# Optimization experiments

Hardware: AMD Instinct MI355X
Metric: run time of the kernel (lower is better)

## Reference

```python
import jax, jax.numpy as jnp
import numpy as np

D_MODEL = 1024

def setup_inputs() -> dict:
    key = jax.random.key(0)
    k1, k2, kU, kb, kw, kfb = jax.random.split(key, 6)
    B, S, d = 8, 2048, D_MODEL
    x1 = jax.random.normal(k1, (B, S, d), dtype=jnp.float32)
    x2 = jax.random.normal(k2, (B, S, d), dtype=jnp.float32)
    U = jax.random.normal(kU, (d, d), dtype=jnp.float32) * (1.0 / np.sqrt(d))
    bias = jax.random.normal(kb, (d,), dtype=jnp.float32) * 0.02
    fc_w = jax.random.normal(kw, (d // 2, d), dtype=jnp.float32) * (1.0 / np.sqrt(d))
    fc_b = jnp.zeros((d // 2,), dtype=jnp.float32)
    return {"x1": x1, "x2": x2, "U": U, "bias": bias, "fc_w": fc_w, "fc_b": fc_b}

def reference(x1, x2, U, bias, fc_w, fc_b):
    # attn scores: (x2 @ U) @ x1^T  -> [B, S2, S1]
    attn = jnp.einsum("bsd,de,bte->bst", x2, U, x1)
    # additive bias per key position: x1 @ bias -> [B, 1, S1]
    attn = attn + jnp.einsum("btd,d->bt", x1, bias)[:, None, :]
    attn = jax.nn.softmax(attn, axis=-1)
    # dropout is identity in eval mode
    out = jnp.einsum("bst,btd->bsd", attn, x1)
    out = jnp.einsum("bsd,ed->bse", out, fc_w) + fc_b
    return jax.nn.relu(out)
```

## Files before the change

### kernel.cpp

```cpp
#include <hip/hip_runtime.h>
#include <hip/hip_fp16.h>
#include <cstddef>
#include <cstdint>

typedef _Float16 f16;
typedef _Float16 f16x8 __attribute__((ext_vector_type(8)));
typedef _Float16 f16x4 __attribute__((ext_vector_type(4)));
typedef float    f32x4 __attribute__((ext_vector_type(4)));

#define BK 64

__device__ __forceinline__ void gload16(const void* g, void* lds) {
  __builtin_amdgcn_global_load_lds(
      (const __attribute__((address_space(1))) unsigned int*)g,
      (__attribute__((address_space(3))) unsigned int*)lds, 16, 0, 0);
}

template<int R>
__device__ __forceinline__ void stage_f16(f16 (*buf)[BK], const f16* __restrict__ src,
                                          int ld, int w, int lane) {
#pragma unroll
  for (int i = 0; i < R / 32; i++) {
    const int grp  = w * (R / 32) + i;
    const int r    = grp * 8 + (lane >> 3);
    const int slot = (lane & 7) ^ (r & 7);
    gload16(src + (size_t)r * ld + slot * 8, &buf[grp * 8][0]);
  }
}

template<int R>
struct RegStage {
  static constexpr int NV = (R == 128) ? 8 : 4;
  float4 v[NV];
  __device__ __forceinline__ void load(const float* __restrict__ src, int ld, int tid) {
    const int r = (R == 128) ? (tid >> 1) : (tid >> 2);
    const int h = (R == 128) ? (tid & 1) * 32 : (tid & 3) * 16;
    const float* p = src + (size_t)r * ld + h;
#pragma unroll
    for (int j = 0; j < NV; j++) v[j] = ((const float4*)p)[j];
  }
  __device__ __forceinline__ void write(f16 (*buf)[BK], int tid) {
    const int r = (R == 128) ? (tid >> 1) : (tid >> 2);
    const int h = (R == 128) ? (tid & 1) * 32 : (tid & 3) * 16;
#pragma unroll
    for (int g = 0; g < NV / 2; g++) {
      const float4 a = v[g * 2], b = v[g * 2 + 1];
      f16x8 o;
      o[0] = (f16)a.x; o[1] = (f16)a.y; o[2] = (f16)a.z; o[3] = (f16)a.w;
      o[4] = (f16)b.x; o[5] = (f16)b.y; o[6] = (f16)b.z; o[7] = (f16)b.w;
      const int slot = (h / 8 + g) ^ (r & 7);
      *(f16x8*)&buf[r][slot * 8] = o;
    }
  }
};

template<int BMt, int BNt, typename TA, typename TB, bool BIAS, bool RELU, typename TC>
__global__ __launch_bounds__(256, 2)
void gemm_tn(const TA* __restrict__ A, int lda,
             const TB* __restrict__ B, int ldb,
             TC* __restrict__ C, int ldc,
             const float* __restrict__ bias, int K)
{
  constexpr int MF = BMt / 32;
  constexpr int NF = BNt / 32;
  __shared__ f16 As[2][BMt][BK];
  __shared__ f16 Bs[2][BNt][BK];
  const int tid  = threadIdx.x;
  const int lane = tid & 63;
  const int w    = tid >> 6;
  const int wr   = w >> 1, wc = w & 1;

  const int gx = gridDim.x, nxy = gx * gridDim.y;
  int lin = blockIdx.y * gx + blockIdx.x;
  lin = (lin & 7) * (nxy >> 3) + (lin >> 3);
  const int m0 = (lin % gx) * BMt;
  const int n0 = (lin / gx) * BNt;

  f32x4 acc[MF][NF] = {};
  RegStage<BMt> ra;
  RegStage<BNt> rb;

  auto stage_issue = [&](int buf, int k0) {
    if constexpr (sizeof(TA) == 2)
      stage_f16<BMt>(As[buf], (const f16*)A + (size_t)m0 * lda + k0, lda, w, lane);
    else
      ra.load((const float*)A + (size_t)m0 * lda + k0, lda, tid);
    if constexpr (sizeof(TB) == 2)
      stage_f16<BNt>(Bs[buf], (const f16*)B + (size_t)n0 * ldb + k0, ldb, w, lane);
    else
      rb.load((const float*)B + (size_t)n0 * ldb + k0, ldb, tid);
  };
  auto stage_write = [&](int buf) {
    if constexpr (sizeof(TA) == 4) ra.write(As[buf], tid);
    if constexpr (sizeof(TB) == 4) rb.write(Bs[buf], tid);
  };
  auto compute = [&](int buf) {
    const int fr = lane & 15, q = lane >> 4;
#pragma unroll
    for (int kk = 0; kk < 2; kk++) {
      f16x8 af[MF], bf[NF];
#pragma unroll
      for (int i = 0; i < MF; i++) {
        const int r = wr * (BMt / 2) + i * 16 + fr;
        const int slot = (kk * 4 + q) ^ (r & 7);
        af[i] = *(const f16x8*)&As[buf][r][slot * 8];
      }
#pragma unroll
      for (int j = 0; j < NF; j++) {
        const int r = wc * (BNt / 2) + j * 16 + fr;
        const int slot = (kk * 4 + q) ^ (r & 7);
        bf[j] = *(const f16x8*)&Bs[buf][r][slot * 8];
      }
#pragma unroll
      for (int i = 0; i < MF; i++)
#pragma unroll
        for (int j = 0; j < NF; j++)
          acc[i][j] = __builtin_amdgcn_mfma_f32_16x16x32_f16(af[i], bf[j], acc[i][j], 0, 0, 0);
    }
  };

  stage_issue(0, 0);
  stage_write(0);
  __syncthreads();

  const int KT = K / BK;
  for (int kt = 0; kt < KT; kt++) {
    const int cur = kt & 1, nxt = cur ^ 1;
    if (kt + 1 < KT) stage_issue(nxt, (kt + 1) * BK);
    compute(cur);
    if (kt + 1 < KT) stage_write(nxt);
    __syncthreads();
  }

  const int fr = lane & 15;
  const int rg = (lane >> 4) << 2;
#pragma unroll
  for (int i = 0; i < MF; i++) {
#pragma unroll
    for (int j = 0; j < NF; j++) {
      const int col = n0 + wc * (BNt / 2) + j * 16 + fr;
      float bv = 0.f;
      if constexpr (BIAS) bv = bias[col];
#pragma unroll
      for (int r = 0; r < 4; r++) {
        const int row = m0 + wr * (BMt / 2) + i * 16 + rg + r;
        float v = acc[i][j][r] + bv;
        if constexpr (RELU) v = fmaxf(v, 0.f);
        C[(size_t)row * ldc + col] = (TC)v;
      }
    }
  }
}

__global__ __launch_bounds__(256)
void copy_f32_f16(const float* __restrict__ in, f16* __restrict__ o)
{
  const size_t i = ((size_t)blockIdx.x * 256 + threadIdx.x) * 8;
  const float4 a = ((const float4*)(in + i))[0];
  const float4 b = ((const float4*)(in + i))[1];
  f16x8 v;
  v[0] = (f16)a.x; v[1] = (f16)a.y; v[2] = (f16)a.z; v[3] = (f16)a.w;
  v[4] = (f16)b.x; v[5] = (f16)b.y; v[6] = (f16)b.z; v[7] = (f16)b.w;
  *(f16x8*)(o + i) = v;
}

__global__ __launch_bounds__(256)
void bias_dot(const float* __restrict__ x1, const float* __restrict__ bias,
              float* __restrict__ bT)
{
  const int row  = blockIdx.x * 4 + (threadIdx.x >> 6);
  const int lane = threadIdx.x & 63;
  const float4* r = (const float4*)(x1 + (size_t)row * 1024);
  const float4* bb = (const float4*)bias;
  float acc = 0.f;
#pragma unroll
  for (int j = 0; j < 4; j++) {
    const float4 a = r[lane + j * 64];
    const float4 b = bb[lane + j * 64];
    acc += a.x * b.x + a.y * b.y + a.z * b.z + a.w * b.w;
  }
#pragma unroll
  for (int off = 32; off > 0; off >>= 1) acc += __shfl_xor(acc, off);
  if (lane == 0) bT[row] = acc;
}

__global__ __launch_bounds__(256)
void softmax_rows(float* __restrict__ S)
{
  float* row = S + (size_t)blockIdx.x * 2048;
  const int t = threadIdx.x;
  const float4 v0 = ((const float4*)row)[t];
  const float4 v1 = ((const float4*)row)[t + 256];

  float m = fmaxf(fmaxf(fmaxf(v0.x, v0.y), fmaxf(v0.z, v0.w)),
                  fmaxf(fmaxf(v1.x, v1.y), fmaxf(v1.z, v1.w)));
#pragma unroll
  for (int off = 32; off > 0; off >>= 1) m = fmaxf(m, __shfl_xor(m, off));
  __shared__ float red[8];
  if ((t & 63) == 0) red[t >> 6] = m;
  __syncthreads();
  m = fmaxf(fmaxf(red[0], red[1]), fmaxf(red[2], red[3]));

  float e0 = __expf(v0.x - m), e1 = __expf(v0.y - m), e2 = __expf(v0.z - m), e3 = __expf(v0.w - m);
  float e4 = __expf(v1.x - m), e5 = __expf(v1.y - m), e6 = __expf(v1.z - m), e7 = __expf(v1.w - m);
  float s = ((e0 + e1) + (e2 + e3)) + ((e4 + e5) + (e6 + e7));
#pragma unroll
  for (int off = 32; off > 0; off >>= 1) s += __shfl_xor(s, off);
  if ((t & 63) == 0) red[4 + (t >> 6)] = s;
  __syncthreads();
  const float inv = 1.f / (red[4] + red[5] + red[6] + red[7]);

  f16x4 o0, o1;
  o0[0] = (f16)(e0 * inv); o0[1] = (f16)(e1 * inv); o0[2] = (f16)(e2 * inv); o0[3] = (f16)(e3 * inv);
  o1[0] = (f16)(e4 * inv); o1[1] = (f16)(e5 * inv); o1[2] = (f16)(e6 * inv); o1[3] = (f16)(e7 * inv);
  f16x4* orow = (f16x4*)row;
  orow[t]       = o0;
  orow[t + 256] = o1;
}

extern "C" void kernel_launch(void* const* d_in, const int* in_sizes, int n_in,
                              void* d_out, int out_size, void* d_ws, size_t ws_size,
                              hipStream_t stream)
{
  const float* x1   = (const float*)d_in[0];
  const float* x2   = (const float*)d_in[1];
  const float* U    = (const float*)d_in[2];
  const float* bias = (const float*)d_in[3];
  const float* fcw  = (const float*)d_in[4];
  const float* fcb  = (const float*)d_in[5];
  float* out = (float*)d_out;

  const int S = 2048, D = 1024, E = 512, B = 8;
  const size_t MB = 1ull << 20;

  char* w = (char*)d_ws;
  f16*   W2  = (f16*)(w);
  f16*   W1T = (f16*)(w + 4 * MB);
  float* bT  = (float*)(w + 6 * MB);
  float* Sb  = (float*)(w + 6 * MB + 256 * 1024);

  const size_t sb_off = 6 * MB + 256 * 1024;
  const int SC = (ws_size >= sb_off + (size_t)S * 2048 * 4) ? 2048 : 1024;

  f16* X2h = (f16*)d_out;

  copy_f32_f16<<<dim3(B * S * D / 2048), 256, 0, stream>>>(x2, X2h);
  bias_dot<<<dim3(B * S / 4), 256, 0, stream>>>(x1, bias, bT);

  for (int b = 0; b < B; b++) {
    const float* x1b = x1 + (size_t)b * S * D;
    const f16*   X2b = X2h + (size_t)b * S * D;

    gemm_tn<64, 128, float, float, false, false, f16><<<dim3(S / 64, D / 128), 256, 0, stream>>>(
        x1b, D, U, D, W2, D, nullptr, D);

    gemm_tn<64, 64, float, float, false, false, f16><<<dim3(E / 64, S / 64), 256, 0, stream>>>(
        fcw, D, x1b, D, W1T, S, nullptr, D);

    for (int s0 = 0; s0 < S; s0 += SC) {
      gemm_tn<64, 128, f16, f16, true, false, float><<<dim3(SC / 64, S / 128), 256, 0, stream>>>(
          X2b + (size_t)s0 * D, D, W2, D, Sb, S, bT + (size_t)b * S, D);
      softmax_rows<<<dim3(SC), 256, 0, stream>>>(Sb);
      gemm_tn<64, 64, f16, f16, true, true, float><<<dim3(SC / 64, E / 64), 256, 0, stream>>>(
          (const f16*)Sb, 2 * S, W1T, S, out + ((size_t)b * S + s0) * E, E, fcb, S);
    }
  }
}
```

Before: 740.0 us.

## Pre-convert all GEMM operands to f16 and use direct LDS loads with BK=128

```diff
diff --git a/kernel.cpp b/kernel.cpp
--- a/kernel.cpp
+++ b/kernel.cpp
@@ -8,63 +8,39 @@
 typedef _Float16 f16x4 __attribute__((ext_vector_type(4)));
 typedef float    f32x4 __attribute__((ext_vector_type(4)));
 
-#define BK 64
-
 __device__ __forceinline__ void gload16(const void* g, void* lds) {
   __builtin_amdgcn_global_load_lds(
       (const __attribute__((address_space(1))) unsigned int*)g,
       (__attribute__((address_space(3))) unsigned int*)lds, 16, 0, 0);
 }
 
-template<int R>
-__device__ __forceinline__ void stage_f16(f16 (*buf)[BK], const f16* __restrict__ src,
+template<int R, int BKt>
+__device__ __forceinline__ void stage_f16(f16 (*buf)[BKt], const f16* __restrict__ src,
                                           int ld, int w, int lane) {
-#pragma unroll
-  for (int i = 0; i < R / 32; i++) {
-    const int grp  = w * (R / 32) + i;
-    const int r    = grp * 8 + (lane >> 3);
-    const int slot = (lane & 7) ^ (r & 7);
-    gload16(src + (size_t)r * ld + slot * 8, &buf[grp * 8][0]);
-  }
-}
-
-template<int R>
-struct RegStage {
-  static constexpr int NV = (R == 128) ? 8 : 4;
-  float4 v[NV];
-  __device__ __forceinline__ void load(const float* __restrict__ src, int ld, int tid) {
-    const int r = (R == 128) ? (tid >> 1) : (tid >> 2);
-    const int h = (R == 128) ? (tid & 1) * 32 : (tid & 3) * 16;
-    const float* p = src + (size_t)r * ld + h;
-#pragma unroll
-    for (int j = 0; j < NV; j++) v[j] = ((const float4*)p)[j];
-  }
-  __device__ __forceinline__ void write(f16 (*buf)[BK], int tid) {
-    const int r = (R == 128) ? (tid >> 1) : (tid >> 2);
-    const int h = (R == 128) ? (tid & 1) * 32 : (tid & 3) * 16;
-#pragma unroll
-    for (int g = 0; g < NV / 2; g++) {
-      const float4 a = v[g * 2], b = v[g * 2 + 1];
-      f16x8 o;
-      o[0] = (f16)a.x; o[1] = (f16)a.y; o[2] = (f16)a.z; o[3] = (f16)a.w;
-      o[4] = (f16)b.x; o[5] = (f16)b.y; o[6] = (f16)b.z; o[7] = (f16)b.w;
-      const int slot = (h / 8 + g) ^ (r & 7);
-      *(f16x8*)&buf[r][slot * 8] = o;
-    }
-  }
-};
-
-template<int BMt, int BNt, typename TA, typename TB, bool BIAS, bool RELU, typename TC>
-__global__ __launch_bounds__(256, 2)
-void gemm_tn(const TA* __restrict__ A, int lda,
-             const TB* __restrict__ B, int ldb,
+  constexpr int RPL = 512 / BKt;
+  constexpr int SPR = BKt / 8;
+  constexpr int LPW = R * BKt / 2048;
+#pragma unroll
+  for (int i = 0; i < LPW; i++) {
+    const int rbase = (w * LPW + i) * RPL;
+    const int r     = rbase + lane / SPR;
+    const int gslot = (lane % SPR) ^ (r & 7);
+    gload16(src + (size_t)r * ld + gslot * 8, &buf[rbase][0]);
+  }
+}
+
+template<int BMt, int BNt, int BKt, bool BIAS, bool RELU, typename TC>
+__global__ __launch_bounds__(256, 1)
+void gemm_tn(const f16* __restrict__ A, int lda,
+             const f16* __restrict__ B, int ldb,
              TC* __restrict__ C, int ldc,
              const float* __restrict__ bias, int K)
 {
   constexpr int MF = BMt / 32;
   constexpr int NF = BNt / 32;
-  __shared__ f16 As[2][BMt][BK];
-  __shared__ f16 Bs[2][BNt][BK];
+  constexpr int KS = BKt / 32;
+  __shared__ f16 As[2][BMt][BKt];
+  __shared__ f16 Bs[2][BNt][BKt];
   const int tid  = threadIdx.x;
   const int lane = tid & 63;
   const int w    = tid >> 6;
@@ -77,27 +53,15 @@
   const int n0 = (lin / gx) * BNt;
 
   f32x4 acc[MF][NF] = {};
-  RegStage<BMt> ra;
-  RegStage<BNt> rb;
-
-  auto stage_issue = [&](int buf, int k0) {
-    if constexpr (sizeof(TA) == 2)
-      stage_f16<BMt>(As[buf], (const f16*)A + (size_t)m0 * lda + k0, lda, w, lane);
-    else
-      ra.load((const float*)A + (size_t)m0 * lda + k0, lda, tid);
-    if constexpr (sizeof(TB) == 2)
-      stage_f16<BNt>(Bs[buf], (const f16*)B + (size_t)n0 * ldb + k0, ldb, w, lane);
-    else
-      rb.load((const float*)B + (size_t)n0 * ldb + k0, ldb, tid);
-  };
-  auto stage_write = [&](int buf) {
-    if constexpr (sizeof(TA) == 4) ra.write(As[buf], tid);
-    if constexpr (sizeof(TB) == 4) rb.write(Bs[buf], tid);
+
+  auto stage = [&](int buf, int k0) {
+    stage_f16<BMt, BKt>(As[buf], A + (size_t)m0 * lda + k0, lda, w, lane);
+    stage_f16<BNt, BKt>(Bs[buf], B + (size_t)n0 * ldb + k0, ldb, w, lane);
   };
   auto compute = [&](int buf) {
     const int fr = lane & 15, q = lane >> 4;
 #pragma unroll
-    for (int kk = 0; kk < 2; kk++) {
+    for (int kk = 0; kk < KS; kk++) {
       f16x8 af[MF], bf[NF];
 #pragma unroll
       for (int i = 0; i < MF; i++) {
@@ -119,16 +83,14 @@
     }
   };
 
-  stage_issue(0, 0);
-  stage_write(0);
+  stage(0, 0);
   __syncthreads();
 
-  const int KT = K / BK;
+  const int KT = K / BKt;
   for (int kt = 0; kt < KT; kt++) {
     const int cur = kt & 1, nxt = cur ^ 1;
-    if (kt + 1 < KT) stage_issue(nxt, (kt + 1) * BK);
+    if (kt + 1 < KT) stage(nxt, (kt + 1) * BKt);
     compute(cur);
-    if (kt + 1 < KT) stage_write(nxt);
     __syncthreads();
   }
 
@@ -231,37 +193,43 @@
   float* out = (float*)d_out;
 
   const int S = 2048, D = 1024, E = 512, B = 8;
+  const int SC = 1024;
   const size_t MB = 1ull << 20;
+  const size_t KB64 = 64 * 1024;
 
   char* w = (char*)d_ws;
   f16*   W2  = (f16*)(w);
   f16*   W1T = (f16*)(w + 4 * MB);
   float* bT  = (float*)(w + 6 * MB);
-  float* Sb  = (float*)(w + 6 * MB + 256 * 1024);
-
-  const size_t sb_off = 6 * MB + 256 * 1024;
-  const int SC = (ws_size >= sb_off + (size_t)S * 2048 * 4) ? 2048 : 1024;
+  float* Sb  = (float*)(w + 6 * MB + KB64);
+  f16*   X1h = (f16*)(w + 6 * MB + KB64);
+  f16*   Uh  = (f16*)(w + 14 * MB + KB64);
+  f16*   Fh  = (f16*)(w + 16 * MB + KB64);
 
   f16* X2h = (f16*)d_out;
 
   copy_f32_f16<<<dim3(B * S * D / 2048), 256, 0, stream>>>(x2, X2h);
+  copy_f32_f16<<<dim3(D * D / 2048), 256, 0, stream>>>(U, Uh);
+  copy_f32_f16<<<dim3(E * D / 2048), 256, 0, stream>>>(fcw, Fh);
   bias_dot<<<dim3(B * S / 4), 256, 0, stream>>>(x1, bias, bT);
 
   for (int b = 0; b < B; b++) {
     const float* x1b = x1 + (size_t)b * S * D;
     const f16*   X2b = X2h + (size_t)b * S * D;
 
-    gemm_tn<64, 128, float, float, false, false, f16><<<dim3(S / 64, D / 128), 256, 0, stream>>>(
-        x1b, D, U, D, W2, D, nullptr, D);
-
-    gemm_tn<64, 64, float, float, false, false, f16><<<dim3(E / 64, S / 64), 256, 0, stream>>>(
-        fcw, D, x1b, D, W1T, S, nullptr, D);
+    copy_f32_f16<<<dim3(S * D / 2048), 256, 0, stream>>>(x1b, X1h);
+
+    gemm_tn<64, 128, 128, false, false, f16><<<dim3(S / 64, D / 128), 256, 0, stream>>>(
+        X1h, D, Uh, D, W2, D, nullptr, D);
+
+    gemm_tn<64, 128, 128, false, false, f16><<<dim3(E / 64, S / 128), 256, 0, stream>>>(
+        Fh, D, X1h, D, W1T, S, nullptr, D);
 
     for (int s0 = 0; s0 < S; s0 += SC) {
-      gemm_tn<64, 128, f16, f16, true, false, float><<<dim3(SC / 64, S / 128), 256, 0, stream>>>(
+      gemm_tn<64, 128, 128, true, false, float><<<dim3(SC / 64, S / 128), 256, 0, stream>>>(
           X2b + (size_t)s0 * D, D, W2, D, Sb, S, bT + (size_t)b * S, D);
       softmax_rows<<<dim3(SC), 256, 0, stream>>>(Sb);
-      gemm_tn<64, 64, f16, f16, true, true, float><<<dim3(SC / 64, E / 64), 256, 0, stream>>>(
+      gemm_tn<64, 64, 128, true, true, float><<<dim3(SC / 64, E / 64), 256, 0, stream>>>(
           (const f16*)Sb, 2 * S, W1T, S, out + ((size_t)b * S + s0) * E, E, fcb, S);
     }
   }
```

Result: slower. 829.2 us (+12.1%).

## Fuse per-batch W2 and W1T GEMMs into one launch with pre-converted f16 weights

Applied to the files above, without the earlier changes.

```diff
diff --git a/kernel.cpp b/kernel.cpp
--- a/kernel.cpp
+++ b/kernel.cpp
@@ -25,6 +25,18 @@
     const int r    = grp * 8 + (lane >> 3);
     const int slot = (lane & 7) ^ (r & 7);
     gload16(src + (size_t)r * ld + slot * 8, &buf[grp * 8][0]);
+  }
+}
+
+template<int R>
+__device__ __forceinline__ void stage_f16p(f16* buf, const f16* __restrict__ src,
+                                           int ld, int w, int lane) {
+#pragma unroll
+  for (int i = 0; i < R / 32; i++) {
+    const int grp  = w * (R / 32) + i;
+    const int r    = grp * 8 + (lane >> 3);
+    const int slot = (lane & 7) ^ (r & 7);
+    gload16(src + (size_t)r * ld + slot * 8, buf + (size_t)grp * 8 * BK);
   }
 }
 
@@ -39,7 +51,7 @@
 #pragma unroll
     for (int j = 0; j < NV; j++) v[j] = ((const float4*)p)[j];
   }
-  __device__ __forceinline__ void write(f16 (*buf)[BK], int tid) {
+  __device__ __forceinline__ void write(f16* buf, int tid) {
     const int r = (R == 128) ? (tid >> 1) : (tid >> 2);
     const int h = (R == 128) ? (tid & 1) * 32 : (tid & 3) * 16;
 #pragma unroll
@@ -49,30 +61,28 @@
       o[0] = (f16)a.x; o[1] = (f16)a.y; o[2] = (f16)a.z; o[3] = (f16)a.w;
       o[4] = (f16)b.x; o[5] = (f16)b.y; o[6] = (f16)b.z; o[7] = (f16)b.w;
       const int slot = (h / 8 + g) ^ (r & 7);
-      *(f16x8*)&buf[r][slot * 8] = o;
+      *(f16x8*)(buf + r * BK + slot * 8) = o;
     }
   }
 };
 
 template<int BMt, int BNt, typename TA, typename TB, bool BIAS, bool RELU, typename TC>
-__global__ __launch_bounds__(256, 2)
-void gemm_tn(const TA* __restrict__ A, int lda,
-             const TB* __restrict__ B, int ldb,
-             TC* __restrict__ C, int ldc,
-             const float* __restrict__ bias, int K)
+__device__ __forceinline__ void gemm_body(char* smem, int lin0, int gx, int nxy,
+                                          const TA* __restrict__ A, int lda,
+                                          const TB* __restrict__ B, int ldb,
+                                          TC* __restrict__ C, int ldc,
+                                          const float* __restrict__ bias, int K)
 {
   constexpr int MF = BMt / 32;
   constexpr int NF = BNt / 32;
-  __shared__ f16 As[2][BMt][BK];
-  __shared__ f16 Bs[2][BNt][BK];
+  f16* AsB = (f16*)smem;
+  f16* BsB = AsB + 2 * BMt * BK;
   const int tid  = threadIdx.x;
   const int lane = tid & 63;
   const int w    = tid >> 6;
   const int wr   = w >> 1, wc = w & 1;
 
-  const int gx = gridDim.x, nxy = gx * gridDim.y;
-  int lin = blockIdx.y * gx + blockIdx.x;
-  lin = (lin & 7) * (nxy >> 3) + (lin >> 3);
+  int lin = (lin0 & 7) * (nxy >> 3) + (lin0 >> 3);
   const int m0 = (lin % gx) * BMt;
   const int n0 = (lin / gx) * BNt;
 
@@ -82,17 +92,17 @@
 
   auto stage_issue = [&](int buf, int k0) {
     if constexpr (sizeof(TA) == 2)
-      stage_f16<BMt>(As[buf], (const f16*)A + (size_t)m0 * lda + k0, lda, w, lane);
+      stage_f16p<BMt>(AsB + buf * BMt * BK, (const f16*)A + (size_t)m0 * lda + k0, lda, w, lane);
     else
       ra.load((const float*)A + (size_t)m0 * lda + k0, lda, tid);
     if constexpr (sizeof(TB) == 2)
-      stage_f16<BNt>(Bs[buf], (const f16*)B + (size_t)n0 * ldb + k0, ldb, w, lane);
+      stage_f16p<BNt>(BsB + buf * BNt * BK, (const f16*)B + (size_t)n0 * ldb + k0, ldb, w, lane);
     else
       rb.load((const float*)B + (size_t)n0 * ldb + k0, ldb, tid);
   };
   auto stage_write = [&](int buf) {
-    if constexpr (sizeof(TA) == 4) ra.write(As[buf], tid);
-    if constexpr (sizeof(TB) == 4) rb.write(Bs[buf], tid);
+    if constexpr (sizeof(TA) == 4) ra.write(AsB + buf * BMt * BK, tid);
+    if constexpr (sizeof(TB) == 4) rb.write(BsB + buf * BNt * BK, tid);
   };
   auto compute = [&](int buf) {
     const int fr = lane & 15, q = lane >> 4;
@@ -103,13 +113,13 @@
       for (int i = 0; i < MF; i++) {
         const int r = wr * (BMt / 2) + i * 16 + fr;
         const int slot = (kk * 4 + q) ^ (r & 7);
-        af[i] = *(const f16x8*)&As[buf][r][slot * 8];
+        af[i] = *(const f16x8*)(AsB + (buf * BMt + r) * BK + slot * 8);
       }
 #pragma unroll
       for (int j = 0; j < NF; j++) {
         const int r = wc * (BNt / 2) + j * 16 + fr;
         const int slot = (kk * 4 + q) ^ (r & 7);
-        bf[j] = *(const f16x8*)&Bs[buf][r][slot * 8];
+        bf[j] = *(const f16x8*)(BsB + (buf * BNt + r) * BK + slot * 8);
       }
 #pragma unroll
       for (int i = 0; i < MF; i++)
@@ -152,6 +162,35 @@
   }
 }
 
+template<int BMt, int BNt, typename TA, typename TB, bool BIAS, bool RELU, typename TC>
+__global__ __launch_bounds__(256, 2)
+void gemm_tn(const TA* __restrict__ A, int lda,
+             const TB* __restrict__ B, int ldb,
+             TC* __restrict__ C, int ldc,
+             const float* __restrict__ bias, int K)
+{
+  __shared__ __align__(16) char smem[2 * (BMt + BNt) * BK * 2];
+  const int nxy = gridDim.x * gridDim.y;
+  gemm_body<BMt, BNt, TA, TB, BIAS, RELU, TC>(
+      smem, blockIdx.y * gridDim.x + blockIdx.x, gridDim.x, nxy,
+      A, lda, B, ldb, C, ldc, bias, K);
+}
+
+__global__ __launch_bounds__(256, 2)
+void k0w1t(const float* __restrict__ x1b, const f16* __restrict__ Uh,
+           const f16* __restrict__ Fh, f16* __restrict__ W2,
+           f16* __restrict__ W1T)
+{
+  __shared__ __align__(16) char smem[2 * (64 + 128) * BK * 2];
+  const int blk = blockIdx.x;
+  if (blk < 256)
+    gemm_body<64, 128, float, f16, false, false, f16>(
+        smem, blk, 32, 256, x1b, 1024, Uh, 1024, W2, 1024, nullptr, 1024);
+  else
+    gemm_body<64, 64, f16, float, false, false, f16>(
+        smem, blk - 256, 8, 256, Fh, 1024, x1b, 1024, W1T, 2048, nullptr, 1024);
+}
+
 __global__ __launch_bounds__(256)
 void copy_f32_f16(const float* __restrict__ in, f16* __restrict__ o)
 {
@@ -165,23 +204,40 @@
 }
 
 __global__ __launch_bounds__(256)
-void bias_dot(const float* __restrict__ x1, const float* __restrict__ bias,
-              float* __restrict__ bT)
-{
-  const int row  = blockIdx.x * 4 + (threadIdx.x >> 6);
-  const int lane = threadIdx.x & 63;
-  const float4* r = (const float4*)(x1 + (size_t)row * 1024);
-  const float4* bb = (const float4*)bias;
-  float acc = 0.f;
-#pragma unroll
-  for (int j = 0; j < 4; j++) {
-    const float4 a = r[lane + j * 64];
-    const float4 b = bb[lane + j * 64];
-    acc += a.x * b.x + a.y * b.y + a.z * b.z + a.w * b.w;
-  }
-#pragma unroll
-  for (int off = 32; off > 0; off >>= 1) acc += __shfl_xor(acc, off);
-  if (lane == 0) bT[row] = acc;
+void prep(const float* __restrict__ x1, const float* __restrict__ bias,
+          float* __restrict__ bT, const float* __restrict__ U,
+          const float* __restrict__ fcw, f16* __restrict__ Uh,
+          f16* __restrict__ Fh)
+{
+  if (blockIdx.x < 4096) {
+    const int row  = blockIdx.x * 4 + (threadIdx.x >> 6);
+    const int lane = threadIdx.x & 63;
+    const float4* r = (const float4*)(x1 + (size_t)row * 1024);
+    const float4* bb = (const float4*)bias;
+    float acc = 0.f;
+#pragma unroll
+    for (int j = 0; j < 4; j++) {
+      const float4 a = r[lane + j * 64];
+      const float4 b = bb[lane + j * 64];
+      acc += a.x * b.x + a.y * b.y + a.z * b.z + a.w * b.w;
+    }
+#pragma unroll
+    for (int off = 32; off > 0; off >>= 1) acc += __shfl_xor(acc, off);
+    if (lane == 0) bT[row] = acc;
+  } else {
+    const int bi = blockIdx.x - 4096;
+    const bool isU = bi < 512;
+    const size_t base = (size_t)(isU ? bi : bi - 512) * 2048;
+    const float* in = (isU ? U : fcw) + base;
+    f16* o = (isU ? Uh : Fh) + base;
+    const size_t i = (size_t)threadIdx.x * 8;
+    const float4 a = ((const float4*)(in + i))[0];
+    const float4 b = ((const float4*)(in + i))[1];
+    f16x8 v;
+    v[0] = (f16)a.x; v[1] = (f16)a.y; v[2] = (f16)a.z; v[3] = (f16)a.w;
+    v[4] = (f16)b.x; v[5] = (f16)b.y; v[6] = (f16)b.z; v[7] = (f16)b.w;
+    *(f16x8*)(o + i) = v;
+  }
 }
 
 __global__ __launch_bounds__(256)
@@ -231,31 +287,28 @@
   float* out = (float*)d_out;
 
   const int S = 2048, D = 1024, E = 512, B = 8;
+  const int SC = 1024;
   const size_t MB = 1ull << 20;
+  const size_t KB64 = 64 * 1024;
 
   char* w = (char*)d_ws;
   f16*   W2  = (f16*)(w);
   f16*   W1T = (f16*)(w + 4 * MB);
   float* bT  = (float*)(w + 6 * MB);
-  float* Sb  = (float*)(w + 6 * MB + 256 * 1024);
-
-  const size_t sb_off = 6 * MB + 256 * 1024;
-  const int SC = (ws_size >= sb_off + (size_t)S * 2048 * 4) ? 2048 : 1024;
+  float* Sb  = (float*)(w + 6 * MB + KB64);
+  f16*   Uh  = (f16*)(w + 14 * MB + KB64);
+  f16*   Fh  = (f16*)(w + 16 * MB + KB64);
 
   f16* X2h = (f16*)d_out;
 
   copy_f32_f16<<<dim3(B * S * D / 2048), 256, 0, stream>>>(x2, X2h);
-  bias_dot<<<dim3(B * S / 4), 256, 0, stream>>>(x1, bias, bT);
+  prep<<<dim3(4864), 256, 0, stream>>>(x1, bias, bT, U, fcw, Uh, Fh);
 
   for (int b = 0; b < B; b++) {
     const float* x1b = x1 + (size_t)b * S * D;
     const f16*   X2b = X2h + (size_t)b * S * D;
 
-    gemm_tn<64, 128, float, float, false, false, f16><<<dim3(S / 64, D / 128), 256, 0, stream>>>(
-        x1b, D, U, D, W2, D, nullptr, D);
-
-    gemm_tn<64, 64, float, float, false, false, f16><<<dim3(E / 64, S / 64), 256, 0, stream>>>(
-        fcw, D, x1b, D, W1T, S, nullptr, D);
+    k0w1t<<<dim3(512), 256, 0, stream>>>(x1b, Uh, Fh, W2, W1T);
 
     for (int s0 = 0; s0 < S; s0 += SC) {
       gemm_tn<64, 128, f16, f16, true, false, float><<<dim3(SC / 64, S / 128), 256, 0, stream>>>(
```

After: 791.5 us. 1.07x slower.
